# Performance work log

Measured on AMD Instinct MI355X. Metric: run time of the kernel, lower is better.

Reference implementation:

```python
import jax, jax.numpy as jnp
import numpy as np

TAU = 2.0      # LIF membrane time constant
EPS = 1e-5     # BatchNorm eps
ALPHA = 4.0    # spikingjelly default Sigmoid surrogate alpha

@jax.custom_vjp
def spike(v):
    return (v >= 0.0).astype(v.dtype)

def _spike_fwd(v):
    return (v >= 0.0).astype(v.dtype), v

def _spike_bwd(v, g):
    s = jax.nn.sigmoid(ALPHA * v)
    return (g * ALPHA * s * (1.0 - s),)

spike.defvjp(_spike_fwd, _spike_bwd)

def lif(x_seq, v_th=1.0):
    # MultiStepLIFNode: v' = v + (x - v)/tau; spike = H(v' - v_th); hard reset to 0 (detach_reset)
    def step(v, x):
        v = v + (x - v) / TAU
        s = spike(v - v_th)
        v = v * (1.0 - jax.lax.stop_gradient(s))
        return v, s
    _, spikes = jax.lax.scan(step, jnp.zeros_like(x_seq[0]), x_seq)
    return spikes

def bn(y, gamma, beta, mean, var, trailing):
    # inference-mode BatchNorm over channel axis 2 of [T,B,C,...]
    shp = (1, 1, -1) + (1,) * trailing
    inv = gamma / jnp.sqrt(var + EPS)
    return (y - mean.reshape(shp)) * inv.reshape(shp) + beta.reshape(shp)

def setup_inputs() -> dict:
    T, B, C, H, W = 4, 32, 512, 16, 16
    key = jax.random.key(0)
    ks = jax.random.split(key, 12)
    return {
        "x": jax.random.normal(ks[0], (T, B, C, H, W), jnp.float32),
        "q_w": jax.random.normal(ks[1], (C, C), jnp.float32) * 0.02,
        "k_w": jax.random.normal(ks[2], (C, C), jnp.float32) * 0.02,
        "v_w": jax.random.normal(ks[3], (C, C), jnp.float32) * 0.02,
        "proj_w": jax.random.normal(ks[4], (C, C), jnp.float32) * 0.02,
        "proj_b": jax.random.normal(ks[5], (C,), jnp.float32) * 0.02,
        "dwc_w": jax.random.normal(ks[6], (C, 1, 5, 5), jnp.float32) * 0.1,
        "dwc_b": jax.random.normal(ks[7], (C,), jnp.float32) * 0.02,
        "bn_gamma": jax.random.uniform(ks[8], (5, C), jnp.float32, 0.5, 1.5),
        "bn_beta": jax.random.normal(ks[9], (5, C), jnp.float32) * 0.1,
        "bn_mean": jax.random.normal(ks[10], (5, C), jnp.float32) * 0.1,
        "bn_var": jax.random.uniform(ks[11], (5, C), jnp.float32, 0.5, 1.5),
    }

def reference(x, q_w, k_w, v_w, proj_w, proj_b, dwc_w, dwc_b,
              bn_gamma, bn_beta, bn_mean, bn_var):
    T, B, C, H, W = x.shape
    num_heads = 8
    d = C // num_heads
    N = H * W
    scale = 0.125
    identity = x

    xs = lif(x).reshape(T, B, C, N)  # spike input, flatten spatial

    def conv_bn(w, idx):
        # 1x1 Conv1d == channel matmul, then inference BN
        y = jnp.einsum('tbcn,dc->tbdn', xs, w)
        return bn(y, bn_gamma[idx], bn_beta[idx], bn_mean[idx], bn_var[idx], 1)

    def to_heads(s):  # [T,B,C,N] -> [T,B,h,N,d]
        return s.reshape(T, B, num_heads, d, N).transpose(0, 1, 2, 4, 3)

    q = to_heads(lif(conv_bn(q_w, 0)))
    k = to_heads(lif(conv_bn(k_w, 1)))
    v = to_heads(lif(conv_bn(v_w, 2)))

    kv = jnp.einsum('tbhnd,tbhne->tbhde', k, v)        # k^T @ v : [d,d] per head
    o = jnp.einsum('tbhnd,tbhde->tbhne', q, kv) * scale  # q @ (kv)
    o = o.transpose(0, 1, 2, 4, 3).reshape(T, B, C, N)

    o = lif(o, v_th=0.5)  # attn_lif with v_threshold=0.5

    y = jnp.einsum('tbcn,dc->tbdn', o, proj_w) + proj_b.reshape(1, 1, -1, 1)
    y = bn(y, bn_gamma[3], bn_beta[3], bn_mean[3], bn_var[3], 1)
    y = y.reshape(T, B, C, H, W)

    z = lif(y).reshape(T * B, C, H, W)
    z = jax.lax.conv_general_dilated(
        z, dwc_w, (1, 1), 'SAME',
        dimension_numbers=('NCHW', 'OIHW', 'NCHW'),
        feature_group_count=C) + dwc_b.reshape(1, -1, 1, 1)
    z = z.reshape(T, B, C, H, W)
    z = bn(z, bn_gamma[4], bn_beta[4], bn_mean[4], bn_var[4], 2)
    return z + identity
```

## Files before the change

### kernel.cpp

```cpp
#include <hip/hip_runtime.h>

#define TT 4
#define BB 32
#define CC 512
#define NN 256
#define DH 64

typedef unsigned char u8;
typedef unsigned short ushort_t;
typedef unsigned int uint_t;
typedef unsigned long long u64;

typedef short bf16x8 __attribute__((ext_vector_type(8)));
typedef float f32x4 __attribute__((ext_vector_type(4)));

static __device__ __forceinline__ unsigned int pack4(unsigned int w){
  return (w & 1u) | ((w >> 7) & 2u) | ((w >> 14) & 4u) | ((w >> 21) & 8u);
}
static __device__ __forceinline__ unsigned int f2bf(float f){
  unsigned int u = __float_as_uint(f);
  return (u + 0x7FFFu + ((u >> 16) & 1u)) >> 16;
}
static __device__ __forceinline__ float bf2f(unsigned int b){
  return __uint_as_float(b << 16);
}

__global__ __launch_bounds__(256) void k_prep(
    const float* __restrict__ qw, const float* __restrict__ kw,
    const float* __restrict__ vw, const float* __restrict__ pw,
    const float* __restrict__ bg, const float* __restrict__ bb,
    const float* __restrict__ bm, const float* __restrict__ bv,
    const float* __restrict__ pb,
    ushort_t* __restrict__ wsp, float* __restrict__ bn2)
{
  int bid = blockIdx.x;
  if (bid < 4096){
    int idx = bid*256 + threadIdx.x;
    int g   = idx >> 18;
    int rem = idx & 262143;
    const float* W = (g==0)? qw : (g==1)? kw : (g==2)? vw : pw;
    float wv = W[rem];
    unsigned int u1 = f2bf(wv);  float r1 = wv - bf2f(u1);
    unsigned int u2 = f2bf(r1);  float r2 = r1 - bf2f(u2);
    unsigned int u3 = f2bf(r2);
    size_t base = (size_t)g*3*262144 + rem;
    wsp[base            ] = (ushort_t)u1;
    wsp[base + 262144   ] = (ushort_t)u2;
    wsp[base + 2*262144 ] = (ushort_t)u3;
  } else {
    for (int i = threadIdx.x; i < 2048; i += 256){
      int g = i >> 9, d = i & 511;
      float inv = bg[g*512+d] / sqrtf(bv[g*512+d] + 1e-5f);
      float bt  = bb[g*512+d] - bm[g*512+d]*inv + ((g==3)? pb[d]*inv : 0.f);
      bn2[i*2+0] = inv;
      bn2[i*2+1] = bt;
    }
  }
}

__global__ __launch_bounds__(256) void k_lif_x(const float* __restrict__ x,
                                               u8* __restrict__ xs){
  const int PL = BB*CC*NN;
  int i = blockIdx.x*256 + threadIdx.x;
  float v = 0.f;
#pragma unroll
  for (int t=0;t<TT;++t){
    float xv = x[(size_t)t*PL + i];
    v = v + (xv - v)*0.5f;
    if (v >= 1.0f){ xs[(size_t)t*PL + i] = 1; v = 0.f; }
    else          { xs[(size_t)t*PL + i] = 0; }
  }
}

__global__ __launch_bounds__(256, 2) void k_gemm_mfma(
    const u8* __restrict__ act, const ushort_t* __restrict__ wsp,
    const float* __restrict__ bn2, u8* __restrict__ out, float vth)
{
  __shared__ __align__(16) ushort_t Alds[3][128][32];
  __shared__ __align__(16) ushort_t Blds[4][4][17][32];

  const int b  = blockIdx.y;
  const int d0 = (blockIdx.x >> 2) * 128;
  const int n0 = (blockIdx.x & 3) * 64;
  const int tid = threadIdx.x;
  const int l   = tid & 63;
  const int wvi = tid >> 6;

  f32x4 acc[2][4][4];
#pragma unroll
  for (int df=0; df<2; ++df)
#pragma unroll
    for (int nf=0; nf<4; ++nf)
#pragma unroll
      for (int t=0; t<4; ++t)
        acc[df][nf][t] = (f32x4){0.f,0.f,0.f,0.f};

  const int ts = tid >> 6;
  const int kp = (tid >> 2) & 15;
  const int nr = tid & 3;
  const int kq = kp >> 2, jj = kp & 3;

  for (int c0 = 0; c0 < CC; c0 += 32){
#pragma unroll
    for (int q=0; q<6; ++q){
      int id = q*256 + tid;
      int s  = id / 512;
      int rm = id & 511;
      int d  = rm >> 2, cc4 = rm & 3;
      const ushort_t* gp = wsp + ((size_t)s*512 + 0)*512
                         + (size_t)(0) ;
      gp = wsp + (size_t)s*262144 + (size_t)(d0 + d)*512 + c0 + cc4*8;
      *(uint4*)&Alds[s][d][cc4*8] = *(const uint4*)gp;
    }
    {
      const u8* sp = act + (((size_t)ts*BB + b)*CC + (c0 + kp*2))*NN + n0 + nr*16;
      uint4 r0 = *(const uint4*)sp;
      uint4 r1 = *(const uint4*)(sp + NN);
      uint_t wa[4] = {r0.x, r0.y, r0.z, r0.w};
      uint_t wb[4] = {r1.x, r1.y, r1.z, r1.w};
#pragma unroll
      for (int c4=0; c4<4; ++c4){
#pragma unroll
        for (int by=0; by<4; ++by){
          int i = c4*4 + by;
          uint_t b0 = (wa[c4] >> (8*by)) & 1u;
          uint_t b1 = (wb[c4] >> (8*by)) & 1u;
          uint_t hv = b0*0x3F80u + b1*0x3F800000u;
          *((uint_t*)&Blds[ts][nr][i][kq*8] + jj) = hv;
        }
      }
    }
    __syncthreads();

    bf16x8 Af[3][2];
#pragma unroll
    for (int s=0; s<3; ++s)
#pragma unroll
      for (int df=0; df<2; ++df)
        Af[s][df] = *(const bf16x8*)&Alds[s][wvi*32 + df*16 + (l&15)][(l>>4)*8];

#pragma unroll
    for (int nf=0; nf<4; ++nf){
      bf16x8 Bf[4];
#pragma unroll
      for (int t=0; t<4; ++t)
        Bf[t] = *(const bf16x8*)&Blds[t][nf][l&15][(l>>4)*8];
#pragma unroll
      for (int s=0; s<3; ++s)
#pragma unroll
        for (int df=0; df<2; ++df)
#pragma unroll
          for (int t=0; t<4; ++t)
            acc[df][nf][t] = __builtin_amdgcn_mfma_f32_16x16x32_bf16(
                Af[s][df], Bf[t], acc[df][nf][t], 0, 0, 0);
    }
    __syncthreads();
  }

#pragma unroll
  for (int df=0; df<2; ++df){
#pragma unroll
    for (int r=0; r<4; ++r){
      int d = d0 + wvi*32 + df*16 + ((l>>4)<<2) + r;
      float inv = bn2[d*2+0], bt = bn2[d*2+1];
#pragma unroll
      for (int nf=0; nf<4; ++nf){
        int n = n0 + nf*16 + (l&15);
        float v = 0.f;
#pragma unroll
        for (int t=0; t<4; ++t){
          float y = acc[df][nf][t][r] * inv + bt;
          v = v + (y - v)*0.5f;
          u8 s = (v >= vth);
          out[(((size_t)t*BB + b)*CC + d)*NN + n] = s;
          if (s) v = 0.f;
        }
      }
    }
  }
}

__global__ __launch_bounds__(256) void k_attn(const u8* __restrict__ qs,
                                              const u8* __restrict__ ks,
                                              const u8* __restrict__ vs,
                                              u8* __restrict__ os)
{
  const int h = blockIdx.x, b = blockIdx.y;
  __shared__ u64 Kb[64][4];
  __shared__ u64 Vb[64][4];
  __shared__ float kvf[64][64];
  const int tid = threadIdx.x;

  float4 vm[16];
#pragma unroll
  for (int e=0;e<16;++e) vm[e] = make_float4(0.f,0.f,0.f,0.f);

  for (int t=0;t<TT;++t){
    size_t base = ((size_t)t*BB + b)*CC*NN + (size_t)h*DH*NN;
#pragma unroll
    for (int p=0;p<4;++p){
      int idx = p*256 + tid;
      int d = idx >> 4;
      int piece = idx & 15;
      uint4 ku = *(const uint4*)(ks + base + (size_t)d*NN + piece*16);
      uint4 vu = *(const uint4*)(vs + base + (size_t)d*NN + piece*16);
      unsigned int kp16 = pack4(ku.x) | (pack4(ku.y)<<4) | (pack4(ku.z)<<8) | (pack4(ku.w)<<12);
      unsigned int vp16 = pack4(vu.x) | (pack4(vu.y)<<4) | (pack4(vu.z)<<8) | (pack4(vu.w)<<12);
      ((unsigned short*)Kb)[d*16 + piece] = (unsigned short)kp16;
      ((unsigned short*)Vb)[d*16 + piece] = (unsigned short)vp16;
    }
    __syncthreads();
    {
      int dd0 = (tid >> 4)*4, ee0 = (tid & 15)*4;
      int cnt[4][4] = {};
#pragma unroll
      for (int wi=0; wi<4; ++wi){
        u64 kw[4], vw[4];
#pragma unroll
        for (int i=0;i<4;++i) kw[i] = Kb[dd0+i][wi];
#pragma unroll
        for (int j=0;j<4;++j) vw[j] = Vb[ee0+j][wi];
#pragma unroll
        for (int i=0;i<4;++i)
#pragma unroll
          for (int j=0;j<4;++j)
            cnt[i][j] += __popcll(kw[i] & vw[j]);
      }
#pragma unroll
      for (int i=0;i<4;++i)
#pragma unroll
        for (int j=0;j<4;++j)
          kvf[dd0+i][ee0+j] = (float)cnt[i][j];
    }
    __syncthreads();
    float4 acc[16];
#pragma unroll
    for (int e=0;e<16;++e) acc[e] = make_float4(0.f,0.f,0.f,0.f);
    const u8* qb = qs + base + tid;
    for (int d=0; d<64; ++d){
      float qf = (float)qb[(size_t)d*NN];
      const float4* kr = (const float4*)&kvf[d][0];
#pragma unroll
      for (int e=0;e<16;++e){
        float4 k4 = kr[e];
        acc[e].x = fmaf(qf, k4.x, acc[e].x);
        acc[e].y = fmaf(qf, k4.y, acc[e].y);
        acc[e].z = fmaf(qf, k4.z, acc[e].z);
        acc[e].w = fmaf(qf, k4.w, acc[e].w);
      }
    }
    u8* ob = os + base + tid;
#pragma unroll
    for (int e=0;e<16;++e){
      float o; u8 s;
      o = acc[e].x*0.125f; vm[e].x += (o - vm[e].x)*0.5f; s = (vm[e].x >= 0.5f); ob[(size_t)(e*4+0)*NN] = s; if (s) vm[e].x = 0.f;
      o = acc[e].y*0.125f; vm[e].y += (o - vm[e].y)*0.5f; s = (vm[e].y >= 0.5f); ob[(size_t)(e*4+1)*NN] = s; if (s) vm[e].y = 0.f;
      o = acc[e].z*0.125f; vm[e].z += (o - vm[e].z)*0.5f; s = (vm[e].z >= 0.5f); ob[(size_t)(e*4+2)*NN] = s; if (s) vm[e].z = 0.f;
      o = acc[e].w*0.125f; vm[e].w += (o - vm[e].w)*0.5f; s = (vm[e].w >= 0.5f); ob[(size_t)(e*4+3)*NN] = s; if (s) vm[e].w = 0.f;
    }
  }
}

__global__ __launch_bounds__(256) void k_dwc(const u8* __restrict__ zs,
                                             const float* __restrict__ x,
                                             const float* __restrict__ dwc_w,
                                             const float* __restrict__ dwc_b,
                                             const float* __restrict__ g4,
                                             const float* __restrict__ b4,
                                             const float* __restrict__ m4,
                                             const float* __restrict__ v4,
                                             float* __restrict__ out)
{
  const int c = blockIdx.x, b = blockIdx.y, t = blockIdx.z;
  __shared__ float zp[20][20];
  __shared__ float wk[25];
  const int tid = threadIdx.x;
  size_t base = (((size_t)t*BB + b)*CC + c)*NN;

  for (int idx = tid; idx < 400; idx += 256){
    int yy = idx/20 - 2, xx = idx%20 - 2;
    float v = 0.f;
    if (yy >= 0 && yy < 16 && xx >= 0 && xx < 16) v = (float)zs[base + yy*16 + xx];
    zp[idx/20][idx%20] = v;
  }
  if (tid < 25) wk[tid] = dwc_w[c*25 + tid];
  __syncthreads();

  const int py = tid >> 4, px = tid & 15;
  float s = 0.f;
#pragma unroll
  for (int i=0;i<5;++i)
#pragma unroll
    for (int j=0;j<5;++j)
      s = fmaf(zp[py+i][px+j], wk[i*5+j], s);
  s += dwc_b[c];
  float inv = g4[c] / sqrtf(v4[c] + 1e-5f);
  float r = (s - m4[c])*inv + b4[c] + x[base + tid];
  out[base + tid] = r;
}

extern "C" void kernel_launch(void* const* d_in, const int* in_sizes, int n_in,
                              void* d_out, int out_size, void* d_ws, size_t ws_size,
                              hipStream_t stream) {
  const float* x      = (const float*)d_in[0];
  const float* q_w    = (const float*)d_in[1];
  const float* k_w    = (const float*)d_in[2];
  const float* v_w    = (const float*)d_in[3];
  const float* proj_w = (const float*)d_in[4];
  const float* proj_b = (const float*)d_in[5];
  const float* dwc_w  = (const float*)d_in[6];
  const float* dwc_b  = (const float*)d_in[7];
  const float* bn_g   = (const float*)d_in[8];
  const float* bn_b   = (const float*)d_in[9];
  const float* bn_m   = (const float*)d_in[10];
  const float* bn_v   = (const float*)d_in[11];
  float* out = (float*)d_out;

  const size_t SZ = (size_t)TT*BB*CC*NN;
  u8* xs  = (u8*)d_ws;
  u8* qs  = xs + SZ;
  u8* ks  = qs + SZ;
  u8* vs  = ks + SZ;
  u8* os  = vs + SZ;
  u8* zsp = os + SZ;
  ushort_t* wsp = (ushort_t*)(zsp + SZ);
  float* bn2    = (float*)(wsp + (size_t)4*3*262144);

  k_prep<<<4097, 256, 0, stream>>>(q_w, k_w, v_w, proj_w,
      bn_g, bn_b, bn_m, bn_v, proj_b, wsp, bn2);

  k_lif_x<<<(BB*CC*NN)/256, 256, 0, stream>>>(x, xs);

  dim3 gg(16, BB);
  k_gemm_mfma<<<gg, 256, 0, stream>>>(xs, wsp + (size_t)0*3*262144, bn2 + 0*1024, qs, 1.0f);
  k_gemm_mfma<<<gg, 256, 0, stream>>>(xs, wsp + (size_t)1*3*262144, bn2 + 1*1024, ks, 1.0f);
  k_gemm_mfma<<<gg, 256, 0, stream>>>(xs, wsp + (size_t)2*3*262144, bn2 + 2*1024, vs, 1.0f);

  k_attn<<<dim3(8, BB), 256, 0, stream>>>(qs, ks, vs, os);

  k_gemm_mfma<<<gg, 256, 0, stream>>>(os, wsp + (size_t)3*3*262144, bn2 + 3*1024, zsp, 1.0f);

  k_dwc<<<dim3(CC, BB, TT), 256, 0, stream>>>(zsp, x, dwc_w, dwc_b,
      bn_g + 4*CC, bn_b + 4*CC, bn_m + 4*CC, bn_v + 4*CC, out);
}
```

Before: 443.2 us.

## Use MFMA for attention q@kv, transposed Q layout, async swizzled weight loads

The q@kv product in the attention kernel moves from scalar FMAs over an fp32 LDS table to bf16 MFMA, with kv stored transposed as bf16 (counts up to 256 are exact in bf16). The Q projection GEMM now writes spikes in a per-head [n][d] layout so attention can load Q fragments directly. Weight tiles are staged via global_load_lds with an XOR swizzle, and the Kb/Vb/Blds LDS arrays are padded to cut bank conflicts. This adds a second epilogue path to the GEMM kernel and relies on the swizzled read indices matching the write layout.

```diff
diff --git a/kernel.cpp b/kernel.cpp
--- a/kernel.cpp
+++ b/kernel.cpp
@@ -13,6 +13,13 @@
 
 typedef short bf16x8 __attribute__((ext_vector_type(8)));
 typedef float f32x4 __attribute__((ext_vector_type(4)));
+
+typedef __attribute__((address_space(1))) const void gv_t;
+typedef __attribute__((address_space(3))) void lv_t;
+
+static __device__ __forceinline__ void gload16(const void* g, void* l){
+  __builtin_amdgcn_global_load_lds((gv_t*)g, (lv_t*)l, 16, 0, 0);
+}
 
 static __device__ __forceinline__ unsigned int pack4(unsigned int w){
   return (w & 1u) | ((w >> 7) & 2u) | ((w >> 14) & 4u) | ((w >> 21) & 8u);
@@ -74,10 +81,11 @@
 
 __global__ __launch_bounds__(256, 2) void k_gemm_mfma(
     const u8* __restrict__ act, const ushort_t* __restrict__ wsp,
-    const float* __restrict__ bn2, u8* __restrict__ out, float vth)
+    const float* __restrict__ bn2, u8* __restrict__ out,
+    u8* __restrict__ out_qt, float vth)
 {
   __shared__ __align__(16) ushort_t Alds[3][128][32];
-  __shared__ __align__(16) ushort_t Blds[4][4][17][32];
+  __shared__ __align__(16) ushort_t Blds[4][4][16][40];
 
   const int b  = blockIdx.y;
   const int d0 = (blockIdx.x >> 2) * 128;
@@ -102,15 +110,14 @@
 
   for (int c0 = 0; c0 < CC; c0 += 32){
 #pragma unroll
-    for (int q=0; q<6; ++q){
-      int id = q*256 + tid;
-      int s  = id / 512;
-      int rm = id & 511;
-      int d  = rm >> 2, cc4 = rm & 3;
-      const ushort_t* gp = wsp + ((size_t)s*512 + 0)*512
-                         + (size_t)(0) ;
-      gp = wsp + (size_t)s*262144 + (size_t)(d0 + d)*512 + c0 + cc4*8;
-      *(uint4*)&Alds[s][d][cc4*8] = *(const uint4*)gp;
+    for (int i=0; i<6; ++i){
+      int id  = i*256 + tid;
+      int s   = id >> 9;
+      int rem = id & 511;
+      int d   = rem >> 2, p = rem & 3;
+      int g   = p ^ ((d + (d>>2)) & 3);
+      const ushort_t* src = wsp + (size_t)s*262144 + (size_t)(d0+d)*512 + c0 + g*8;
+      gload16(src, (ushort_t*)Alds + (size_t)id*8);
     }
     {
       const u8* sp = act + (((size_t)ts*BB + b)*CC + (c0 + kp*2))*NN + n0 + nr*16;
@@ -136,8 +143,11 @@
 #pragma unroll
     for (int s=0; s<3; ++s)
 #pragma unroll
-      for (int df=0; df<2; ++df)
-        Af[s][df] = *(const bf16x8*)&Alds[s][wvi*32 + df*16 + (l&15)][(l>>4)*8];
+      for (int df=0; df<2; ++df){
+        int row = wvi*32 + df*16 + (l&15);
+        int pc  = (l>>4) ^ ((row + (row>>2)) & 3);
+        Af[s][df] = *(const bf16x8*)&Alds[s][row][pc*8];
+      }
 
 #pragma unroll
     for (int nf=0; nf<4; ++nf){
@@ -157,46 +167,97 @@
     __syncthreads();
   }
 
-#pragma unroll
-  for (int df=0; df<2; ++df){
-#pragma unroll
-    for (int r=0; r<4; ++r){
-      int d = d0 + wvi*32 + df*16 + ((l>>4)<<2) + r;
-      float inv = bn2[d*2+0], bt = bn2[d*2+1];
+  if (out_qt){
+#pragma unroll
+    for (int df=0; df<2; ++df){
+      int dbase = d0 + wvi*32 + df*16 + ((l>>4)<<2);
+      int h = dbase >> 6, dh = dbase & 63;
+      float inv4[4], bt4[4];
+#pragma unroll
+      for (int r=0;r<4;++r){ inv4[r] = bn2[(dbase+r)*2]; bt4[r] = bn2[(dbase+r)*2+1]; }
 #pragma unroll
       for (int nf=0; nf<4; ++nf){
         int n = n0 + nf*16 + (l&15);
-        float v = 0.f;
+        float vm0=0.f, vm1=0.f, vm2=0.f, vm3=0.f;
 #pragma unroll
         for (int t=0; t<4; ++t){
-          float y = acc[df][nf][t][r] * inv + bt;
-          v = v + (y - v)*0.5f;
-          u8 s = (v >= vth);
-          out[(((size_t)t*BB + b)*CC + d)*NN + n] = s;
-          if (s) v = 0.f;
+          uchar4 sv;
+          float y0 = acc[df][nf][t][0]*inv4[0] + bt4[0];
+          vm0 = vm0 + (y0 - vm0)*0.5f; sv.x = (vm0 >= vth); if (sv.x) vm0 = 0.f;
+          float y1 = acc[df][nf][t][1]*inv4[1] + bt4[1];
+          vm1 = vm1 + (y1 - vm1)*0.5f; sv.y = (vm1 >= vth); if (sv.y) vm1 = 0.f;
+          float y2 = acc[df][nf][t][2]*inv4[2] + bt4[2];
+          vm2 = vm2 + (y2 - vm2)*0.5f; sv.z = (vm2 >= vth); if (sv.z) vm2 = 0.f;
+          float y3 = acc[df][nf][t][3]*inv4[3] + bt4[3];
+          vm3 = vm3 + (y3 - vm3)*0.5f; sv.w = (vm3 >= vth); if (sv.w) vm3 = 0.f;
+          *(uchar4*)(out_qt + ((((size_t)t*BB + b)*8 + h)*256 + n)*64 + dh) = sv;
         }
       }
     }
-  }
-}
-
-__global__ __launch_bounds__(256) void k_attn(const u8* __restrict__ qs,
-                                              const u8* __restrict__ ks,
-                                              const u8* __restrict__ vs,
-                                              u8* __restrict__ os)
+  } else {
+#pragma unroll
+    for (int df=0; df<2; ++df){
+#pragma unroll
+      for (int r=0; r<4; ++r){
+        int d = d0 + wvi*32 + df*16 + ((l>>4)<<2) + r;
+        float inv = bn2[d*2+0], bt = bn2[d*2+1];
+#pragma unroll
+        for (int nf=0; nf<4; ++nf){
+          int n = n0 + nf*16 + (l&15);
+          float v = 0.f;
+#pragma unroll
+          for (int t=0; t<4; ++t){
+            float y = acc[df][nf][t][r] * inv + bt;
+            v = v + (y - v)*0.5f;
+            u8 s = (v >= vth);
+            out[(((size_t)t*BB + b)*CC + d)*NN + n] = s;
+            if (s) v = 0.f;
+          }
+        }
+      }
+    }
+  }
+}
+
+__global__ __launch_bounds__(256, 1) void k_attn(const u8* __restrict__ qt,
+                                                 const u8* __restrict__ ks,
+                                                 const u8* __restrict__ vs,
+                                                 u8* __restrict__ os)
 {
   const int h = blockIdx.x, b = blockIdx.y;
-  __shared__ u64 Kb[64][4];
-  __shared__ u64 Vb[64][4];
-  __shared__ float kvf[64][64];
+  __shared__ u64 Kb[64][5];
+  __shared__ u64 Vb[64][5];
+  __shared__ __align__(16) ushort_t kvbf[64][88];
   const int tid = threadIdx.x;
-
-  float4 vm[16];
-#pragma unroll
-  for (int e=0;e<16;++e) vm[e] = make_float4(0.f,0.f,0.f,0.f);
+  const int l   = tid & 63;
+  const int wvi = tid >> 6;
+
+  f32x4 vm[4][4];
+#pragma unroll
+  for (int nf=0;nf<4;++nf)
+#pragma unroll
+    for (int ef=0;ef<4;++ef) vm[nf][ef] = (f32x4){0.f,0.f,0.f,0.f};
 
   for (int t=0;t<TT;++t){
-    size_t base = ((size_t)t*BB + b)*CC*NN + (size_t)h*DH*NN;
+    size_t base  = ((size_t)t*BB + b)*CC*NN + (size_t)h*DH*NN;
+    const u8* qtb = qt + (((size_t)t*BB + b)*8 + h)*256*64;
+
+    bf16x8 aq[4][2];
+#pragma unroll
+    for (int nf=0; nf<4; ++nf){
+      int n = wvi*64 + nf*16 + (l&15);
+#pragma unroll
+      for (int kf=0; kf<2; ++kf){
+        uint2 qu = *(const uint2*)(qtb + (size_t)n*64 + kf*32 + (l>>4)*8);
+        union { uint_t u[4]; bf16x8 v; } cv;
+        cv.u[0] = (qu.x & 1u)*0x3F80u + ((qu.x >> 8) & 1u)*0x3F800000u;
+        cv.u[1] = ((qu.x >> 16) & 1u)*0x3F80u + ((qu.x >> 24) & 1u)*0x3F800000u;
+        cv.u[2] = (qu.y & 1u)*0x3F80u + ((qu.y >> 8) & 1u)*0x3F800000u;
+        cv.u[3] = ((qu.y >> 16) & 1u)*0x3F80u + ((qu.y >> 24) & 1u)*0x3F800000u;
+        aq[nf][kf] = cv.v;
+      }
+    }
+
 #pragma unroll
     for (int p=0;p<4;++p){
       int idx = p*256 + tid;
@@ -206,10 +267,11 @@
       uint4 vu = *(const uint4*)(vs + base + (size_t)d*NN + piece*16);
       unsigned int kp16 = pack4(ku.x) | (pack4(ku.y)<<4) | (pack4(ku.z)<<8) | (pack4(ku.w)<<12);
       unsigned int vp16 = pack4(vu.x) | (pack4(vu.y)<<4) | (pack4(vu.z)<<8) | (pack4(vu.w)<<12);
-      ((unsigned short*)Kb)[d*16 + piece] = (unsigned short)kp16;
-      ((unsigned short*)Vb)[d*16 + piece] = (unsigned short)vp16;
+      ((ushort_t*)Kb)[d*20 + piece] = (ushort_t)kp16;
+      ((ushort_t*)Vb)[d*20 + piece] = (ushort_t)vp16;
     }
     __syncthreads();
+
     {
       int dd0 = (tid >> 4)*4, ee0 = (tid & 15)*4;
       int cnt[4][4] = {};
@@ -230,34 +292,49 @@
       for (int i=0;i<4;++i)
 #pragma unroll
         for (int j=0;j<4;++j)
-          kvf[dd0+i][ee0+j] = (float)cnt[i][j];
+          kvbf[ee0+j][dd0+i] = (ushort_t)(__float_as_uint((float)cnt[i][j]) >> 16);
     }
     __syncthreads();
-    float4 acc[16];
-#pragma unroll
-    for (int e=0;e<16;++e) acc[e] = make_float4(0.f,0.f,0.f,0.f);
-    const u8* qb = qs + base + tid;
-    for (int d=0; d<64; ++d){
-      float qf = (float)qb[(size_t)d*NN];
-      const float4* kr = (const float4*)&kvf[d][0];
-#pragma unroll
-      for (int e=0;e<16;++e){
-        float4 k4 = kr[e];
-        acc[e].x = fmaf(qf, k4.x, acc[e].x);
-        acc[e].y = fmaf(qf, k4.y, acc[e].y);
-        acc[e].z = fmaf(qf, k4.z, acc[e].z);
-        acc[e].w = fmaf(qf, k4.w, acc[e].w);
-      }
-    }
-    u8* ob = os + base + tid;
-#pragma unroll
-    for (int e=0;e<16;++e){
-      float o; u8 s;
-      o = acc[e].x*0.125f; vm[e].x += (o - vm[e].x)*0.5f; s = (vm[e].x >= 0.5f); ob[(size_t)(e*4+0)*NN] = s; if (s) vm[e].x = 0.f;
-      o = acc[e].y*0.125f; vm[e].y += (o - vm[e].y)*0.5f; s = (vm[e].y >= 0.5f); ob[(size_t)(e*4+1)*NN] = s; if (s) vm[e].y = 0.f;
-      o = acc[e].z*0.125f; vm[e].z += (o - vm[e].z)*0.5f; s = (vm[e].z >= 0.5f); ob[(size_t)(e*4+2)*NN] = s; if (s) vm[e].z = 0.f;
-      o = acc[e].w*0.125f; vm[e].w += (o - vm[e].w)*0.5f; s = (vm[e].w >= 0.5f); ob[(size_t)(e*4+3)*NN] = s; if (s) vm[e].w = 0.f;
-    }
+
+    f32x4 acc[4][4];
+#pragma unroll
+    for (int nf=0;nf<4;++nf)
+#pragma unroll
+      for (int ef=0;ef<4;++ef) acc[nf][ef] = (f32x4){0.f,0.f,0.f,0.f};
+
+#pragma unroll
+    for (int ef=0; ef<4; ++ef){
+      bf16x8 bv[2];
+#pragma unroll
+      for (int kf=0; kf<2; ++kf)
+        bv[kf] = *(const bf16x8*)&kvbf[ef*16 + (l&15)][kf*32 + (l>>4)*8];
+#pragma unroll
+      for (int nf=0; nf<4; ++nf)
+#pragma unroll
+        for (int kf=0; kf<2; ++kf)
+          acc[nf][ef] = __builtin_amdgcn_mfma_f32_16x16x32_bf16(
+              aq[nf][kf], bv[kf], acc[nf][ef], 0, 0, 0);
+    }
+
+#pragma unroll
+    for (int nf=0; nf<4; ++nf){
+#pragma unroll
+      for (int ef=0; ef<4; ++ef){
+        int e = ef*16 + (l&15);
+        int n4 = wvi*64 + nf*16 + ((l>>4)<<2);
+        uchar4 sv;
+        float o0 = acc[nf][ef][0]*0.125f;
+        vm[nf][ef][0] += (o0 - vm[nf][ef][0])*0.5f; sv.x = (vm[nf][ef][0] >= 0.5f); if (sv.x) vm[nf][ef][0] = 0.f;
+        float o1 = acc[nf][ef][1]*0.125f;
+        vm[nf][ef][1] += (o1 - vm[nf][ef][1])*0.5f; sv.y = (vm[nf][ef][1] >= 0.5f); if (sv.y) vm[nf][ef][1] = 0.f;
+        float o2 = acc[nf][ef][2]*0.125f;
+        vm[nf][ef][2] += (o2 - vm[nf][ef][2])*0.5f; sv.z = (vm[nf][ef][2] >= 0.5f); if (sv.z) vm[nf][ef][2] = 0.f;
+        float o3 = acc[nf][ef][3]*0.125f;
+        vm[nf][ef][3] += (o3 - vm[nf][ef][3])*0.5f; sv.w = (vm[nf][ef][3] >= 0.5f); if (sv.w) vm[nf][ef][3] = 0.f;
+        *(uchar4*)(os + base + (size_t)e*NN + n4) = sv;
+      }
+    }
+    __syncthreads();
   }
 }
 
@@ -318,8 +395,8 @@
 
   const size_t SZ = (size_t)TT*BB*CC*NN;
   u8* xs  = (u8*)d_ws;
-  u8* qs  = xs + SZ;
-  u8* ks  = qs + SZ;
+  u8* qtp = xs + SZ;
+  u8* ks  = qtp + SZ;
   u8* vs  = ks + SZ;
   u8* os  = vs + SZ;
   u8* zsp = os + SZ;
@@ -332,13 +409,13 @@
   k_lif_x<<<(BB*CC*NN)/256, 256, 0, stream>>>(x, xs);
 
   dim3 gg(16, BB);
-  k_gemm_mfma<<<gg, 256, 0, stream>>>(xs, wsp + (size_t)0*3*262144, bn2 + 0*1024, qs, 1.0f);
-  k_gemm_mfma<<<gg, 256, 0, stream>>>(xs, wsp + (size_t)1*3*262144, bn2 + 1*1024, ks, 1.0f);
-  k_gemm_mfma<<<gg, 256, 0, stream>>>(xs, wsp + (size_t)2*3*262144, bn2 + 2*1024, vs, 1.0f);
-
-  k_attn<<<dim3(8, BB), 256, 0, stream>>>(qs, ks, vs, os);
-
-  k_gemm_mfma<<<gg, 256, 0, stream>>>(os, wsp + (size_t)3*3*262144, bn2 + 3*1024, zsp, 1.0f);
+  k_gemm_mfma<<<gg, 256, 0, stream>>>(xs, wsp + (size_t)0*3*262144, bn2 + 0*1024, nullptr, qtp, 1.0f);
+  k_gemm_mfma<<<gg, 256, 0, stream>>>(xs, wsp + (size_t)1*3*262144, bn2 + 1*1024, ks, nullptr, 1.0f);
+  k_gemm_mfma<<<gg, 256, 0, stream>>>(xs, wsp + (size_t)2*3*262144, bn2 + 2*1024, vs, nullptr, 1.0f);
+
+  k_attn<<<dim3(8, BB), 256, 0, stream>>>(qtp, ks, vs, os);
+
+  k_gemm_mfma<<<gg, 256, 0, stream>>>(os, wsp + (size_t)3*3*262144, bn2 + 3*1024, zsp, nullptr, 1.0f);
 
   k_dwc<<<dim3(CC, BB, TT), 256, 0, stream>>>(zsp, x, dwc_w, dwc_b,
       bn_g + 4*CC, bn_b + 4*CC, bn_m + 4*CC, bn_v + 4*CC, out);
```

After: 408.5 us. 1.08x faster.
